# Kernel optimization log

Measured on AMD Instinct MI355X. Metric: run time of the kernel, lower is better.

The kernel has to match this reference:

```python
import jax, jax.numpy as jnp
import numpy as np

DIM = 128
DIM_HEAD = 32
HEADS = 4
B, H, W = 4, 256, 256
NSCALE = 4  # M=1, nScale=4 hardcoded in New_msa's gaborT
KS = 7


def _gabor_dw_weight(dim):
    # torch.arange(-7//2, 7//2) -> [-4, ..., 2] (7 values), indexing 'ij'
    coords = jnp.arange(-(KS // 2) - 1, KS // 2, dtype=jnp.float32)
    xm, ym = jnp.meshgrid(coords, coords, indexing='ij')
    freqs = (0.1 + 0.6 * jnp.arange(NSCALE, dtype=jnp.float32) / (NSCALE - 1)) / 2.0
    # theta = 0 (M=1): x_theta = xm, y_theta = ym; sigma = 1
    k = jnp.exp(-(xm[None] ** 2 + (ym[None] / freqs[:, None, None]) ** 2) / 2.0)  # [4,7,7]
    w = jnp.tile(k, (dim, 1, 1))[:, None]  # [dim*4, 1, 7, 7], weight.repeat(dim,1,1,1)
    return w


def setup_inputs() -> dict:
    key = jax.random.key(0)
    ks = jax.random.split(key, 8)
    s = 1.0 / np.sqrt(DIM)
    inner = DIM_HEAD * HEADS
    return {
        'x_in': jax.random.normal(ks[0], (B, H, W, DIM), jnp.float32),
        'Wq': jax.random.normal(ks[1], (DIM, inner), jnp.float32) * s,
        'Wk': jax.random.normal(ks[2], (DIM, inner), jnp.float32) * s,
        'Wv': jax.random.normal(ks[3], (DIM, inner), jnp.float32) * s,
        'rescale': jnp.ones((HEADS, 1, 1), jnp.float32),
        'Wproj': jax.random.normal(ks[4], (inner, DIM), jnp.float32) * s,
        'bproj': jnp.zeros((DIM,), jnp.float32),
        'dw_w': _gabor_dw_weight(DIM),
        'dw_b': jax.random.normal(ks[5], (DIM * NSCALE,), jnp.float32) * 0.01,
        'pw_w': jax.random.normal(ks[6], (DIM, DIM * NSCALE), jnp.float32) / np.sqrt(DIM * NSCALE),
        'pw_b': jnp.zeros((DIM,), jnp.float32),
    }


def _l2norm(t, eps=1e-12):
    # F.normalize(p=2, dim=-1): x / max(||x||, eps)
    return t / jnp.maximum(jnp.linalg.norm(t, axis=-1, keepdims=True), eps)


def reference(x_in, Wq, Wk, Wv, rescale, Wproj, bproj, dw_w, dw_b, pw_w, pw_b):
    b, h, w, c = x_in.shape
    n = h * w
    heads, d = HEADS, DIM_HEAD
    x = x_in.reshape(b, n, c)
    v_inp = x @ Wv  # [b, n, heads*d]
    # [b, n, hd] -> [b, heads, d, n] (channel-wise attention)
    to_hdn = lambda t: t.reshape(b, n, heads, d).transpose(0, 2, 3, 1)
    q = _l2norm(to_hdn(x @ Wq))
    k = _l2norm(to_hdn(x @ Wk))
    v = to_hdn(v_inp)
    attn = jnp.einsum('bhdn,bhen->bhde', k, q) * rescale  # [b, heads, d, d]
    attn = jax.nn.softmax(attn, axis=-1)
    o = jnp.einsum('bhde,bhen->bhdn', attn, v)
    o = o.transpose(0, 3, 1, 2).reshape(b, n, heads * d)
    out_c = (o @ Wproj + bproj).reshape(b, h, w, c)
    v_img = v_inp.reshape(b, h, w, c).transpose(0, 3, 1, 2)  # NCHW
    g = jax.lax.conv_general_dilated(
        v_img, dw_w, window_strides=(1, 1), padding=[(KS // 2, KS // 2)] * 2,
        dimension_numbers=('NCHW', 'OIHW', 'NCHW'), feature_group_count=c)
    g = jax.nn.gelu(g + dw_b[None, :, None, None], approximate=False)
    out_p = jnp.einsum('oc,bchw->bohw', pw_w, g) + pw_b[None, :, None, None]
    return out_c + out_p.transpose(0, 2, 3, 1)
```

## Files before the change

kernel.cpp:

```cpp
#include <hip/hip_runtime.h>


using bf16x8 = __attribute__((ext_vector_type(8))) short;
using f32x4  = __attribute__((ext_vector_type(4))) float;

__device__ __forceinline__ unsigned short f2bf(float f) {
  __bf16 h = (__bf16)f;
  return __builtin_bit_cast(unsigned short, h);
}
__device__ __forceinline__ float bf2f(unsigned short u) {
  union { unsigned u; float f; } v; v.u = ((unsigned)u) << 16;
  return v.f;
}
__device__ __forceinline__ float gelu_f(float x) {
  float u = 0.7978845608028654f * (x + 0.044715f * x * x * x);
  float e = __expf(2.0f * u);
  float th = 1.0f - 2.0f * __builtin_amdgcn_rcpf(e + 1.0f);
  return 0.5f * x * (1.0f + th);
}

__global__ void k_prep(const float* __restrict__ pw, unsigned short* __restrict__ pwb,
                       float* __restrict__ S) {
  int blk = blockIdx.x;
  if (blk < 256) { int idx = blk * 256 + threadIdx.x; pwb[idx] = f2bf(pw[idx]); }
  else           { int idx = (blk - 256) * 256 + threadIdx.x; S[idx] = 0.f; }
}

__global__ __launch_bounds__(256, 2) void k_vgram(
    const float* __restrict__ x, const float* __restrict__ Wv,
    unsigned short* __restrict__ vout, float* __restrict__ partial) {
  __shared__ unsigned short WvT[128 * 128];
  __shared__ unsigned short xs [64 * 128];
  __shared__ unsigned short xsT[128 * 64];
  char* WvT_c = (char*)WvT; char* xs_c = (char*)xs; char* xsT_c = (char*)xsT;
  const int tid = threadIdx.x;
  const int bid = blockIdx.x;
  const int b = bid >> 7;
  const long n0 = (long)(bid & 127) * 512;
  const float* __restrict__ xb = x + (long)b * 65536 * 128;

  {
    int c = tid >> 1;
    int o0 = (tid & 1) * 64;
    const float* src = Wv + c * 128 + o0;
    #pragma unroll
    for (int u = 0; u < 64; u += 4) {
      float4 w = *(const float4*)(src + u);
      unsigned short q0 = f2bf(w.x), q1 = f2bf(w.y), q2 = f2bf(w.z), q3 = f2bf(w.w);
      int o = o0 + u;
      *(unsigned short*)(WvT_c + (o + 0) * 256 + ((2 * c) ^ (((o + 0) & 7) << 4))) = q0;
      *(unsigned short*)(WvT_c + (o + 1) * 256 + ((2 * c) ^ (((o + 1) & 7) << 4))) = q1;
      *(unsigned short*)(WvT_c + (o + 2) * 256 + ((2 * c) ^ (((o + 2) & 7) << 4))) = q2;
      *(unsigned short*)(WvT_c + (o + 3) * 256 + ((2 * c) ^ (((o + 3) & 7) << 4))) = q3;
    }
  }
  __syncthreads();

  const int wave = tid >> 6, lane = tid & 63;
  const int quad = lane >> 4, l16 = lane & 15;
  const int swl = (l16 & 7) << 4;

  f32x4 accg[2][8];
  #pragma unroll
  for (int i = 0; i < 2; ++i)
    #pragma unroll
    for (int nt = 0; nt < 8; ++nt) accg[i][nt] = (f32x4){0.f, 0.f, 0.f, 0.f};

  for (int so = 0; so < 8; ++so) {
    const long r0 = n0 + so * 64;
    {
      int row = tid >> 2;
      int c0 = (tid & 3) * 32;
      const float* src = xb + (r0 + row) * 128 + c0;
      char* xrow = xs_c + row * 256;
      const int sw = (row & 7) << 4;
      #pragma unroll
      for (int u = 0; u < 32; u += 4) {
        float4 t = *(const float4*)(src + u);
        ushort4 p;
        p.x = f2bf(t.x); p.y = f2bf(t.y); p.z = f2bf(t.z); p.w = f2bf(t.w);
        int c = c0 + u;
        *(ushort4*)(xrow + ((2 * c) ^ sw)) = p;
        *(unsigned short*)(xsT_c + (c + 0) * 128 + ((2 * row) ^ (((c + 0) & 7) << 4))) = p.x;
        *(unsigned short*)(xsT_c + (c + 1) * 128 + ((2 * row) ^ (((c + 1) & 7) << 4))) = p.y;
        *(unsigned short*)(xsT_c + (c + 2) * 128 + ((2 * row) ^ (((c + 2) & 7) << 4))) = p.z;
        *(unsigned short*)(xsT_c + (c + 3) * 128 + ((2 * row) ^ (((c + 3) & 7) << 4))) = p.w;
      }
    }
    __syncthreads();

    f32x4 accv[8];
    #pragma unroll
    for (int nt = 0; nt < 8; ++nt) accv[nt] = (f32x4){0.f, 0.f, 0.f, 0.f};
    #pragma unroll
    for (int ks = 0; ks < 4; ++ks) {
      bf16x8 af = *(const bf16x8*)(xs_c + (16 * wave + l16) * 256 +
                                   ((64 * ks + 16 * quad) ^ swl));
      #pragma unroll
      for (int nt = 0; nt < 8; ++nt) {
        bf16x8 bfr = *(const bf16x8*)(WvT_c + (16 * nt + l16) * 256 +
                                      ((64 * ks + 16 * quad) ^ swl));
        accv[nt] = __builtin_amdgcn_mfma_f32_16x16x32_bf16(af, bfr, accv[nt], 0, 0, 0);
      }
    }
    {
      long rbase = (long)b * 65536 + r0 + 16 * wave + 4 * quad;
      #pragma unroll
      for (int nt = 0; nt < 8; ++nt)
        #pragma unroll
        for (int r = 0; r < 4; ++r)
          vout[(rbase + r) * 128 + 16 * nt + l16] = f2bf(accv[nt][r]);
    }

    #pragma unroll
    for (int ks = 0; ks < 2; ++ks) {
      bf16x8 fr[8];
      bf16x8 fa0, fa1;
      #pragma unroll
      for (int t8 = 0; t8 < 8; ++t8) {
        int cc = 16 * t8 + l16;
        bf16x8 f = *(const bf16x8*)(xsT_c + cc * 128 + ((64 * ks + 16 * quad) ^ swl));
        fr[t8] = f;
        if (t8 == 2 * wave)     fa0 = f;
        if (t8 == 2 * wave + 1) fa1 = f;
      }
      #pragma unroll
      for (int nt = 0; nt < 8; ++nt) {
        accg[0][nt] = __builtin_amdgcn_mfma_f32_16x16x32_bf16(fa0, fr[nt], accg[0][nt], 0, 0, 0);
        accg[1][nt] = __builtin_amdgcn_mfma_f32_16x16x32_bf16(fa1, fr[nt], accg[1][nt], 0, 0, 0);
      }
    }
    __syncthreads();
  }

  {
    float* pp = partial + (long)bid * 16384;
    #pragma unroll
    for (int i = 0; i < 2; ++i) {
      int mr = 16 * (2 * wave + i) + 4 * quad;
      #pragma unroll
      for (int nt = 0; nt < 8; ++nt)
        #pragma unroll
        for (int r = 0; r < 4; ++r)
          pp[(mr + r) * 128 + 16 * nt + l16] = accg[i][nt][r];
    }
  }
}

__global__ void k_reduce(const float* __restrict__ partial, float* __restrict__ S) {
  int t = blockIdx.x * 256 + threadIdx.x;
  int idx = t & 65535;
  int kg  = t >> 16;
  int bb = idx >> 14;
  int ij = idx & 16383;
  const float* p = partial + (long)bb * (128L * 16384) + (long)kg * (32L * 16384) + ij;
  float s = 0.f;
  #pragma unroll 4
  for (int k = 0; k < 32; ++k) s += p[(long)k * 16384];
  atomicAdd(S + idx, s);
}

__global__ __launch_bounds__(256) void k_attn(
    const float* __restrict__ S, const float* __restrict__ Wq,
    const float* __restrict__ Wk, const float* __restrict__ rescale,
    const float* __restrict__ Wproj, unsigned short* __restrict__ W2T) {
  __shared__ float Ssf[64 * 128];
  __shared__ float Tq[128][32];
  __shared__ float G[32][33];
  __shared__ float attnS[32][33];
  __shared__ float nq[32];
  __shared__ float nkp[8][32];
  const int tid = threadIdx.x;
  const int b = blockIdx.x >> 2;
  const int h = blockIdx.x & 3;
  const float* Sb = S + b * 16384;
  const int e = tid & 31, ig = tid >> 5, col = 32 * h + e;

  {
    float nk_s = 0.f;
    for (int cb = 0; cb < 2; ++cb) {
      __syncthreads();
      #pragma unroll
      for (int u = 0; u < 8; ++u) {
        int idx = u * 1024 + tid * 4;
        *(float4*)&Ssf[idx] = *(const float4*)(Sb + cb * 8192 + idx);
      }
      __syncthreads();
      float aq[8], ak[8];
      #pragma unroll
      for (int m = 0; m < 8; ++m) { aq[m] = 0.f; ak[m] = 0.f; }
      for (int j = 0; j < 128; ++j) {
        float wq = Wq[j * 128 + col];
        float wk = Wk[j * 128 + col];
        #pragma unroll
        for (int m = 0; m < 8; ++m) {
          float s = Ssf[(ig + 8 * m) * 128 + j];
          aq[m] += s * wq;
          ak[m] += s * wk;
        }
      }
      #pragma unroll
      for (int m = 0; m < 8; ++m) {
        int i = 64 * cb + ig + 8 * m;
        Tq[i][e] = aq[m];
        nk_s += Wk[i * 128 + col] * ak[m];
      }
    }
    nkp[ig][e] = nk_s;
  }
  __syncthreads();
  {
    int d0 = ig * 4;
    float g[4] = {0.f, 0.f, 0.f, 0.f};
    for (int i = 0; i < 128; ++i) {
      float tq = Tq[i][e];
      #pragma unroll
      for (int d = 0; d < 4; ++d) g[d] += Wk[i * 128 + 32 * h + d0 + d] * tq;
    }
    #pragma unroll
    for (int d = 0; d < 4; ++d) G[d0 + d][e] = g[d];
  }
  if (tid < 32) {
    float s = 0.f;
    for (int i = 0; i < 128; ++i) s += Wq[i * 128 + col] * Tq[i][tid];
    nq[tid] = s;
  }
  __syncthreads();
  if (tid < 32) {
    int d = tid;
    float nk_d = 0.f;
    #pragma unroll
    for (int g2 = 0; g2 < 8; ++g2) nk_d += nkp[g2][d];
    float rsc = rescale[h];
    float rk = fmaxf(sqrtf(fmaxf(nk_d, 0.f)), 1e-12f);
    float L[32];
    float mx = -3.4e38f;
    #pragma unroll
    for (int e2 = 0; e2 < 32; ++e2) {
      float rq = fmaxf(sqrtf(fmaxf(nq[e2], 0.f)), 1e-12f);
      float l = G[d][e2] * rsc / (rk * rq);
      L[e2] = l;
      mx = fmaxf(mx, l);
    }
    float sum = 0.f;
    #pragma unroll
    for (int e2 = 0; e2 < 32; ++e2) {
      float p = __expf(L[e2] - mx);
      attnS[d][e2] = p;
      sum += p;
    }
    float inv = 1.0f / sum;
    #pragma unroll
    for (int e2 = 0; e2 < 32; ++e2) attnS[d][e2] *= inv;
  }
  __syncthreads();
  {
    int co = tid & 127;
    int e0 = (tid >> 7) * 16;
    float s[16];
    #pragma unroll
    for (int e2 = 0; e2 < 16; ++e2) s[e2] = 0.f;
    for (int d = 0; d < 32; ++d) {
      float wp = Wproj[(32 * h + d) * 128 + co];
      #pragma unroll
      for (int e2 = 0; e2 < 16; ++e2) s[e2] += attnS[d][e0 + e2] * wp;
    }
    #pragma unroll
    for (int e2 = 0; e2 < 16; ++e2)
      W2T[((long)b * 128 + co) * 128 + 32 * h + e0 + e2] = f2bf(s[e2]);
  }
}

__global__ __launch_bounds__(256, 3) void k_final(
    const unsigned short* __restrict__ v, const unsigned short* __restrict__ W2T,
    const unsigned short* __restrict__ pwb, const float* __restrict__ dw_w,
    const float* __restrict__ dw_b, const float* __restrict__ bproj,
    const float* __restrict__ pw_b, float* __restrict__ out) {
  __shared__ unsigned short t_lds[8 * 14 * 128];
  __shared__ unsigned short A_lds[64 * 64];
  __shared__ unsigned short B_lds[128 * 64];
  char* t_c = (char*)t_lds; char* A_c = (char*)A_lds; char* B_c = (char*)B_lds;
  const int tid = threadIdx.x;
  const int bid0 = blockIdx.x;
  const int bid = (bid0 & 7) * 512 + (bid0 >> 3);
  const int b = bid >> 10;
  const int tile = bid & 1023;
  const int y0 = (tile >> 5) * 8;
  const int x0 = (tile & 31) * 8;

  float a_[7];
  #pragma unroll
  for (int i = 0; i < 7; ++i) a_[i] = dw_w[i * 7 + 4];
  float bco[4][7];
  #pragma unroll
  for (int s = 0; s < 4; ++s)
    #pragma unroll
    for (int j = 0; j < 7; ++j) bco[s][j] = dw_w[s * 49 + 28 + j];

  #pragma unroll
  for (int it = 0; it < 2; ++it) {
    int colid = tid + 256 * it;
    if (colid < 448) {
      int xh = colid >> 5;
      int c4 = (colid & 31) * 4;
      int xg = x0 + xh - 3;
      bool inx = (xg >= 0) && (xg < 256);
      float rows_[14][4];
      #pragma unroll
      for (int yy = 0; yy < 14; ++yy) {
        int yg = y0 + yy - 3;
        float f0 = 0.f, f1 = 0.f, f2 = 0.f, f3 = 0.f;
        if (inx && yg >= 0 && yg < 256) {
          ushort4 vv = *(const ushort4*)&v[((long)b * 65536 + yg * 256 + xg) * 128 + c4];
          f0 = bf2f(vv.x); f1 = bf2f(vv.y); f2 = bf2f(vv.z); f3 = bf2f(vv.w);
        }
        rows_[yy][0] = f0; rows_[yy][1] = f1; rows_[yy][2] = f2; rows_[yy][3] = f3;
      }
      #pragma unroll
      for (int yl = 0; yl < 8; ++yl) {
        float t0 = 0.f, t1 = 0.f, t2 = 0.f, t3 = 0.f;
        #pragma unroll
        for (int i = 0; i < 7; ++i) {
          float w = a_[i];
          t0 += w * rows_[yl + i][0];
          t1 += w * rows_[yl + i][1];
          t2 += w * rows_[yl + i][2];
          t3 += w * rows_[yl + i][3];
        }
        ushort4 p; p.x = f2bf(t0); p.y = f2bf(t1); p.z = f2bf(t2); p.w = f2bf(t3);
        int trow = yl * 14 + xh;
        *(ushort4*)(t_c + trow * 256 + ((2 * c4) ^ ((trow & 15) << 4))) = p;
      }
    }
  }
  __syncthreads();

  const int wave = tid >> 6, lane = tid & 63;
  const int quad = lane >> 4, l16 = lane & 15;
  const int swl = (l16 & 7) << 4;
  f32x4 acc[8];
  #pragma unroll
  for (int nt = 0; nt < 8; ++nt) acc[nt] = (f32x4){0.f, 0.f, 0.f, 0.f};

  for (int kc = 0; kc < 10; ++kc) {
    {
      int o = tid >> 1;
      int k0 = (tid & 1) * 32;
      const unsigned short* src = (kc < 2)
          ? (W2T + ((long)b * 128 + o) * 128 + kc * 64 + k0)
          : (pwb + (long)o * 512 + (kc - 2) * 64 + k0);
      const int sw = (o & 7) << 4;
      #pragma unroll
      for (int u = 0; u < 32; u += 8)
        *(uint4*)(B_c + o * 128 + ((2 * (k0 + u)) ^ sw)) = *(const uint4*)(src + u);
    }
    if (kc < 2) {
      int pix = tid >> 2;
      int c0 = (tid & 3) * 16;
      const unsigned short* src =
          v + ((long)b * 65536 + (y0 + (pix >> 3)) * 256 + x0 + (pix & 7)) * 128 + kc * 64 + c0;
      const int sw = (pix & 7) << 4;
      *(uint4*)(A_c + pix * 128 + ((2 * c0) ^ sw))      = *(const uint4*)(src);
      *(uint4*)(A_c + pix * 128 + ((2 * c0 + 16) ^ sw)) = *(const uint4*)(src + 8);
    } else {
      int kcg = kc - 2;
      int pix = tid >> 2;
      int cl = (tid & 3) * 4;
      int yl = pix >> 3, xl = pix & 7;
      float tv[7][4];
      #pragma unroll
      for (int j = 0; j < 7; ++j) {
        int trow = yl * 14 + xl + j;
        ushort4 tt = *(const ushort4*)(t_c + trow * 256 +
                                       ((32 * kcg + 2 * cl) ^ ((trow & 15) << 4)));
        tv[j][0] = bf2f(tt.x); tv[j][1] = bf2f(tt.y); tv[j][2] = bf2f(tt.z); tv[j][3] = bf2f(tt.w);
      }
      const int sw = (pix & 7) << 4;
      #pragma unroll
      for (int cc = 0; cc < 4; ++cc) {
        int ch = (16 * kcg + cl + cc) * 4;
        unsigned short gs[4];
        #pragma unroll
        for (int s = 0; s < 4; ++s) {
          float g = dw_b[ch + s];
          #pragma unroll
          for (int j = 0; j < 7; ++j) g += bco[s][j] * tv[j][cc];
          gs[s] = f2bf(gelu_f(g));
        }
        ushort4 p; p.x = gs[0]; p.y = gs[1]; p.z = gs[2]; p.w = gs[3];
        *(ushort4*)(A_c + pix * 128 + ((8 * (cl + cc)) ^ sw)) = p;
      }
    }
    __syncthreads();
    #pragma unroll
    for (int ks = 0; ks < 2; ++ks) {
      bf16x8 af = *(const bf16x8*)(A_c + (16 * wave + l16) * 128 +
                                   ((64 * ks + 16 * quad) ^ swl));
      #pragma unroll
      for (int nt = 0; nt < 8; ++nt) {
        bf16x8 bfr = *(const bf16x8*)(B_c + (16 * nt + l16) * 128 +
                                      ((64 * ks + 16 * quad) ^ swl));
        acc[nt] = __builtin_amdgcn_mfma_f32_16x16x32_bf16(af, bfr, acc[nt], 0, 0, 0);
      }
    }
    __syncthreads();
  }

  int mr = 16 * wave + 4 * quad;
  #pragma unroll
  for (int nt = 0; nt < 8; ++nt) {
    int col = 16 * nt + l16;
    float bias = bproj[col] + pw_b[col];
    #pragma unroll
    for (int r = 0; r < 4; ++r) {
      int pix = mr + r;
      out[((long)b * 65536 + (y0 + (pix >> 3)) * 256 + x0 + (pix & 7)) * 128 + col] =
          acc[nt][r] + bias;
    }
  }
}

extern "C" void kernel_launch(void* const* d_in, const int* in_sizes, int n_in,
                              void* d_out, int out_size, void* d_ws, size_t ws_size,
                              hipStream_t stream) {
  const float* x       = (const float*)d_in[0];
  const float* Wq      = (const float*)d_in[1];
  const float* Wk      = (const float*)d_in[2];
  const float* Wv      = (const float*)d_in[3];
  const float* rescale = (const float*)d_in[4];
  const float* Wproj   = (const float*)d_in[5];
  const float* bproj   = (const float*)d_in[6];
  const float* dw_w    = (const float*)d_in[7];
  const float* dw_b    = (const float*)d_in[8];
  const float* pw_w    = (const float*)d_in[9];
  const float* pw_b    = (const float*)d_in[10];
  float* out = (float*)d_out;

  char* ws = (char*)d_ws;
  unsigned short* v       = (unsigned short*)(ws);
  float*          partial = (float*)(ws + 67108864);
  float*          S       = (float*)(ws + 100663296);
  unsigned short* W2T     = (unsigned short*)(ws + 100925440);
  unsigned short* pwb     = (unsigned short*)(ws + 101056512);

  k_prep  <<<512, 256, 0, stream>>>(pw_w, pwb, S);
  k_vgram <<<512, 256, 0, stream>>>(x, Wv, v, partial);
  k_reduce<<<1024,256, 0, stream>>>(partial, S);
  k_attn  <<<16,  256, 0, stream>>>(S, Wq, Wk, rescale, Wproj, W2T);
  k_final <<<4096,256, 0, stream>>>(v, W2T, pwb, dw_w, dw_b, bproj, pw_b, out);
}
```

Before: 460.2 us.

## Split final-kernel vertical conv into halves, stage Wq/Wk in LDS, pack v stores

Several changes land together. k_final now runs the vertical depthwise pass in two 64-channel halves interleaved with the K loop, which roughly halves the t_lds buffer (padded rows, no swizzle) and raises launch bounds to 4 blocks per SM. The v-projection output is written as packed ushort2 pairs after a lane shuffle instead of scalar 16-bit stores. A new xsT swizzle reduces LDS bank conflicts, k_attn stages its Wq/Wk head slices in shared memory, and GELU is rewritten as a sigmoid form with fewer operations. The extra __syncthreads inside the K loop and the higher occupancy target may cost registers or stall time.

```diff
diff --git a/kernel.cpp b/kernel.cpp
--- a/kernel.cpp
+++ b/kernel.cpp
@@ -13,10 +13,13 @@
   return v.f;
 }
 __device__ __forceinline__ float gelu_f(float x) {
-  float u = 0.7978845608028654f * (x + 0.044715f * x * x * x);
-  float e = __expf(2.0f * u);
-  float th = 1.0f - 2.0f * __builtin_amdgcn_rcpf(e + 1.0f);
-  return 0.5f * x * (1.0f + th);
+  float x2 = x * x;
+  float y = x * fmaf(0.0713548162726f, x2, 1.5957691216057308f);
+  float e = __expf(-y);
+  return x * __builtin_amdgcn_rcpf(1.0f + e);
+}
+__device__ __forceinline__ int swz_xsT(int c) {
+  return ((c ^ (c >> 3) ^ (c >> 6)) & 7) << 4;
 }
 
 __global__ void k_prep(const float* __restrict__ pw, unsigned short* __restrict__ pwb,
@@ -81,10 +84,10 @@
         p.x = f2bf(t.x); p.y = f2bf(t.y); p.z = f2bf(t.z); p.w = f2bf(t.w);
         int c = c0 + u;
         *(ushort4*)(xrow + ((2 * c) ^ sw)) = p;
-        *(unsigned short*)(xsT_c + (c + 0) * 128 + ((2 * row) ^ (((c + 0) & 7) << 4))) = p.x;
-        *(unsigned short*)(xsT_c + (c + 1) * 128 + ((2 * row) ^ (((c + 1) & 7) << 4))) = p.y;
-        *(unsigned short*)(xsT_c + (c + 2) * 128 + ((2 * row) ^ (((c + 2) & 7) << 4))) = p.z;
-        *(unsigned short*)(xsT_c + (c + 3) * 128 + ((2 * row) ^ (((c + 3) & 7) << 4))) = p.w;
+        *(unsigned short*)(xsT_c + (c + 0) * 128 + ((2 * row) ^ swz_xsT(c + 0))) = p.x;
+        *(unsigned short*)(xsT_c + (c + 1) * 128 + ((2 * row) ^ swz_xsT(c + 1))) = p.y;
+        *(unsigned short*)(xsT_c + (c + 2) * 128 + ((2 * row) ^ swz_xsT(c + 2))) = p.z;
+        *(unsigned short*)(xsT_c + (c + 3) * 128 + ((2 * row) ^ swz_xsT(c + 3))) = p.w;
       }
     }
     __syncthreads();
@@ -105,11 +108,21 @@
     }
     {
       long rbase = (long)b * 65536 + r0 + 16 * wave + 4 * quad;
-      #pragma unroll
-      for (int nt = 0; nt < 8; ++nt)
+      const int odd = lane & 1;
+      const int colb = (l16 & ~1);
+      #pragma unroll
+      for (int nt = 0; nt < 8; ++nt) {
         #pragma unroll
-        for (int r = 0; r < 4; ++r)
-          vout[(rbase + r) * 128 + 16 * nt + l16] = f2bf(accv[nt][r]);
+        for (int rp = 0; rp < 4; rp += 2) {
+          float xg = __shfl_xor(accv[nt][rp], 1, 64);
+          float yg = __shfl_xor(accv[nt][rp + 1], 1, 64);
+          float lo = odd ? yg : accv[nt][rp];
+          float hi = odd ? accv[nt][rp + 1] : xg;
+          ushort2 pk; pk.x = f2bf(lo); pk.y = f2bf(hi);
+          long row = rbase + rp + odd;
+          *(ushort2*)&vout[row * 128 + 16 * nt + colb] = pk;
+        }
+      }
     }
 
     #pragma unroll
@@ -119,7 +132,7 @@
       #pragma unroll
       for (int t8 = 0; t8 < 8; ++t8) {
         int cc = 16 * t8 + l16;
-        bf16x8 f = *(const bf16x8*)(xsT_c + cc * 128 + ((64 * ks + 16 * quad) ^ swl));
+        bf16x8 f = *(const bf16x8*)(xsT_c + cc * 128 + ((64 * ks + 16 * quad) ^ swz_xsT(cc)));
         fr[t8] = f;
         if (t8 == 2 * wave)     fa0 = f;
         if (t8 == 2 * wave + 1) fa1 = f;
@@ -166,6 +179,8 @@
     const float* __restrict__ Wproj, unsigned short* __restrict__ W2T) {
   __shared__ float Ssf[64 * 128];
   __shared__ float Tq[128][32];
+  __shared__ float WqL[128][32];
+  __shared__ float WkL[128][32];
   __shared__ float G[32][33];
   __shared__ float attnS[32][33];
   __shared__ float nq[32];
@@ -174,7 +189,19 @@
   const int b = blockIdx.x >> 2;
   const int h = blockIdx.x & 3;
   const float* Sb = S + b * 16384;
-  const int e = tid & 31, ig = tid >> 5, col = 32 * h + e;
+  const int e = tid & 31, ig = tid >> 5;
+
+  {
+    int j = tid >> 1;
+    int c0 = (tid & 1) * 16;
+    const float* sq = Wq + j * 128 + 32 * h + c0;
+    const float* sk = Wk + j * 128 + 32 * h + c0;
+    #pragma unroll
+    for (int u = 0; u < 16; u += 4) {
+      *(float4*)&WqL[j][c0 + u] = *(const float4*)(sq + u);
+      *(float4*)&WkL[j][c0 + u] = *(const float4*)(sk + u);
+    }
+  }
 
   {
     float nk_s = 0.f;
@@ -190,8 +217,8 @@
       #pragma unroll
       for (int m = 0; m < 8; ++m) { aq[m] = 0.f; ak[m] = 0.f; }
       for (int j = 0; j < 128; ++j) {
-        float wq = Wq[j * 128 + col];
-        float wk = Wk[j * 128 + col];
+        float wq = WqL[j][e];
+        float wk = WkL[j][e];
         #pragma unroll
         for (int m = 0; m < 8; ++m) {
           float s = Ssf[(ig + 8 * m) * 128 + j];
@@ -203,7 +230,7 @@
       for (int m = 0; m < 8; ++m) {
         int i = 64 * cb + ig + 8 * m;
         Tq[i][e] = aq[m];
-        nk_s += Wk[i * 128 + col] * ak[m];
+        nk_s += WkL[i][e] * ak[m];
       }
     }
     nkp[ig][e] = nk_s;
@@ -215,14 +242,14 @@
     for (int i = 0; i < 128; ++i) {
       float tq = Tq[i][e];
       #pragma unroll
-      for (int d = 0; d < 4; ++d) g[d] += Wk[i * 128 + 32 * h + d0 + d] * tq;
+      for (int d = 0; d < 4; ++d) g[d] += WkL[i][d0 + d] * tq;
     }
     #pragma unroll
     for (int d = 0; d < 4; ++d) G[d0 + d][e] = g[d];
   }
   if (tid < 32) {
     float s = 0.f;
-    for (int i = 0; i < 128; ++i) s += Wq[i * 128 + col] * Tq[i][tid];
+    for (int i = 0; i < 128; ++i) s += WqL[i][tid] * Tq[i][tid];
     nq[tid] = s;
   }
   __syncthreads();
@@ -271,15 +298,15 @@
   }
 }
 
-__global__ __launch_bounds__(256, 3) void k_final(
+__global__ __launch_bounds__(256, 4) void k_final(
     const unsigned short* __restrict__ v, const unsigned short* __restrict__ W2T,
     const unsigned short* __restrict__ pwb, const float* __restrict__ dw_w,
     const float* __restrict__ dw_b, const float* __restrict__ bproj,
     const float* __restrict__ pw_b, float* __restrict__ out) {
-  __shared__ unsigned short t_lds[8 * 14 * 128];
+  __shared__ unsigned short t_lds[112 * 72];
   __shared__ unsigned short A_lds[64 * 64];
   __shared__ unsigned short B_lds[128 * 64];
-  char* t_c = (char*)t_lds; char* A_c = (char*)A_lds; char* B_c = (char*)B_lds;
+  char* A_c = (char*)A_lds; char* B_c = (char*)B_lds;
   const int tid = threadIdx.x;
   const int bid0 = blockIdx.x;
   const int bid = (bid0 & 7) * 512 + (bid0 >> 3);
@@ -297,12 +324,11 @@
     #pragma unroll
     for (int j = 0; j < 7; ++j) bco[s][j] = dw_w[s * 49 + 28 + j];
 
-  #pragma unroll
-  for (int it = 0; it < 2; ++it) {
-    int colid = tid + 256 * it;
-    if (colid < 448) {
-      int xh = colid >> 5;
-      int c4 = (colid & 31) * 4;
+  auto vertical = [&](int hf) {
+    if (tid < 224) {
+      int xh = tid >> 4;
+      int cl = (tid & 15) * 4;
+      int cg = 64 * hf + cl;
       int xg = x0 + xh - 3;
       bool inx = (xg >= 0) && (xg < 256);
       float rows_[14][4];
@@ -311,7 +337,7 @@
         int yg = y0 + yy - 3;
         float f0 = 0.f, f1 = 0.f, f2 = 0.f, f3 = 0.f;
         if (inx && yg >= 0 && yg < 256) {
-          ushort4 vv = *(const ushort4*)&v[((long)b * 65536 + yg * 256 + xg) * 128 + c4];
+          ushort4 vv = *(const ushort4*)&v[((long)b * 65536 + yg * 256 + xg) * 128 + cg];
           f0 = bf2f(vv.x); f1 = bf2f(vv.y); f2 = bf2f(vv.z); f3 = bf2f(vv.w);
         }
         rows_[yy][0] = f0; rows_[yy][1] = f1; rows_[yy][2] = f2; rows_[yy][3] = f3;
@@ -328,12 +354,10 @@
           t3 += w * rows_[yl + i][3];
         }
         ushort4 p; p.x = f2bf(t0); p.y = f2bf(t1); p.z = f2bf(t2); p.w = f2bf(t3);
-        int trow = yl * 14 + xh;
-        *(ushort4*)(t_c + trow * 256 + ((2 * c4) ^ ((trow & 15) << 4))) = p;
-      }
-    }
-  }
-  __syncthreads();
+        *(ushort4*)&t_lds[(yl * 14 + xh) * 72 + cl] = p;
+      }
+    }
+  };
 
   const int wave = tid >> 6, lane = tid & 63;
   const int quad = lane >> 4, l16 = lane & 15;
@@ -343,6 +367,8 @@
   for (int nt = 0; nt < 8; ++nt) acc[nt] = (f32x4){0.f, 0.f, 0.f, 0.f};
 
   for (int kc = 0; kc < 10; ++kc) {
+    if (kc == 2) { vertical(0); __syncthreads(); }
+    if (kc == 6) { vertical(1); __syncthreads(); }
     {
       int o = tid >> 1;
       int k0 = (tid & 1) * 32;
@@ -364,6 +390,7 @@
       *(uint4*)(A_c + pix * 128 + ((2 * c0 + 16) ^ sw)) = *(const uint4*)(src + 8);
     } else {
       int kcg = kc - 2;
+      int kcl = kcg & 3;
       int pix = tid >> 2;
       int cl = (tid & 3) * 4;
       int yl = pix >> 3, xl = pix & 7;
@@ -371,8 +398,7 @@
       #pragma unroll
       for (int j = 0; j < 7; ++j) {
         int trow = yl * 14 + xl + j;
-        ushort4 tt = *(const ushort4*)(t_c + trow * 256 +
-                                       ((32 * kcg + 2 * cl) ^ ((trow & 15) << 4)));
+        ushort4 tt = *(const ushort4*)&t_lds[trow * 72 + 16 * kcl + cl];
         tv[j][0] = bf2f(tt.x); tv[j][1] = bf2f(tt.y); tv[j][2] = bf2f(tt.z); tv[j][3] = bf2f(tt.w);
       }
       const int sw = (pix & 7) << 4;
```

Measured after the change: 494.5 us. 7.5% more time.
